# Optimization experiments

Hardware: AMD Instinct MI355X
Metric: run time of the kernel (lower is better)

The kernel has to match this reference:

```python
import jax, jax.numpy as jnp
import numpy as np

NUM_ANCHORS = 400_000
NUM_GTS = 64
NUM_CLASSES = 1
TOPK = 10
ALPHA = 1.0
BETA = 6.0
IMG = 640.0


def setup_inputs() -> dict:
    key = jax.random.key(0)
    k1, k2, k3, k4, k5, k6 = jax.random.split(key, 6)
    # anchor points uniformly over the image plane
    anc_points = jax.random.uniform(k1, (NUM_ANCHORS, 2), jnp.float32, 0.0, IMG)
    # predicted boxes: centered near the anchor point, valid xyxy
    pd_wh = jax.random.uniform(k2, (NUM_ANCHORS, 2), jnp.float32, 8.0, 96.0)
    pd_bboxes = jnp.concatenate([anc_points - pd_wh * 0.5, anc_points + pd_wh * 0.5], axis=-1)
    # predicted class scores in [0, 1] (post-sigmoid)
    pd_scores = jax.random.uniform(k3, (NUM_ANCHORS, NUM_CLASSES), jnp.float32)
    # GT boxes: random centers / sizes, valid xyxy
    gt_c = jax.random.uniform(k4, (NUM_GTS, 2), jnp.float32, 64.0, IMG - 64.0)
    gt_wh = jax.random.uniform(k5, (NUM_GTS, 2), jnp.float32, 16.0, 128.0)
    gt_bboxes = jnp.concatenate([gt_c - gt_wh * 0.5, gt_c + gt_wh * 0.5], axis=-1)
    gt_labels = jax.random.randint(k6, (NUM_GTS,), 0, NUM_CLASSES, dtype=jnp.int32)
    return {
        "pd_scores": pd_scores,
        "pd_bboxes": pd_bboxes,
        "anc_points": anc_points,
        "gt_labels": gt_labels,
        "gt_bboxes": gt_bboxes,
    }


def _box_iou(b1, b2):
    # b1: [A,4] xyxy, b2: [G,4] xyxy -> [A,G] pairwise IoU (torchvision box_iou math)
    lt = jnp.maximum(b1[:, None, :2], b2[None, :, :2])  # [A,G,2]
    rb = jnp.minimum(b1[:, None, 2:], b2[None, :, 2:])  # [A,G,2]
    wh = jnp.clip(rb - lt, 0.0)
    inter = wh[..., 0] * wh[..., 1]                      # [A,G]
    area1 = (b1[:, 2] - b1[:, 0]) * (b1[:, 3] - b1[:, 1])
    area2 = (b2[:, 2] - b2[:, 0]) * (b2[:, 3] - b2[:, 1])
    return inter / (area1[:, None] + area2[None, :] - inter)


def reference(pd_scores, pd_bboxes, anc_points, gt_labels, gt_bboxes):
    A = anc_points.shape[0]
    G = gt_bboxes.shape[0]
    # is anchor point inside each GT box -> [A,G] bool
    x, y = anc_points[:, 0:1], anc_points[:, 1:2]
    is_in_gts = ((x >= gt_bboxes[None, :, 0]) & (x <= gt_bboxes[None, :, 2]) &
                 (y >= gt_bboxes[None, :, 1]) & (y <= gt_bboxes[None, :, 3]))
    # Original gathers candidate anchors (inside >=1 GT) then computes metrics.
    # Equivalent dense form: non-candidates have is_in_gts row all-False so their
    # alignment metric is 0 for every GT and they are filtered by metric>0 below.
    iou = _box_iou(pd_bboxes, gt_bboxes)                         # [A,G]
    cls_scores = pd_scores[:, gt_labels]                          # [A,G]
    cls_scores = cls_scores * is_in_gts.astype(cls_scores.dtype)
    metric = (cls_scores ** ALPHA) * (iou ** BETA)                # [A,G]
    # per-GT top-k anchors by alignment metric
    _, topk_idx = jax.lax.top_k(metric.T, TOPK)                   # [G,k]
    topk_mask = jnp.zeros((A, G), dtype=bool)
    topk_mask = topk_mask.at[topk_idx.T, jnp.arange(G)[None, :]].set(True)
    topk_mask = topk_mask & (metric > 0)
    is_assigned = topk_mask.any(axis=1)                           # [A]
    best_gt = jnp.argmax(metric, axis=1)                          # [A]
    fg_mask = is_assigned
    assigned_gt_idx = jnp.where(fg_mask, best_gt, 0).astype(jnp.int32)
    return fg_mask, assigned_gt_idx
```

## Files before the change

### kernel.cpp

```cpp
#include <hip/hip_runtime.h>

#define NUM_A    400000
#define NUM_G    64
#define TOPK     10
#define CHUNKS   64
#define CHUNK_SZ (NUM_A / CHUNKS)
#define GGROUP   4
#define NGROUPS  (NUM_G / GGROUP)
#define CAP      768
#define SENT_I   0x7fffffff

__device__ __forceinline__ bool better(float m1, int a1, float m2, int a2) {
    return (m1 > m2) || ((m1 == m2) && (a1 < a2));
}

__device__ __forceinline__ float iou_metric(
    float px1, float py1, float px2, float py2, float parea, float score,
    float gx1, float gy1, float gx2, float gy2, float garea)
{
    float ltx = fmaxf(px1, gx1);
    float lty = fmaxf(py1, gy1);
    float rbx = fminf(px2, gx2);
    float rby = fminf(py2, gy2);
    float w = fmaxf(rbx - ltx, 0.0f);
    float h = fmaxf(rby - lty, 0.0f);
    float inter = w * h;
    float iou = inter / (parea + garea - inter);
    float iou2 = iou * iou;
    float iou6 = iou2 * iou2 * iou2;
    return score * iou6;
}

__device__ __forceinline__ void wave_max_pair(float& bv, int& bi) {
#pragma unroll
    for (int s = 1; s < 64; s <<= 1) {
        float ov = __shfl_xor(bv, s, 64);
        int   oi = __shfl_xor(bi, s, 64);
        if (better(ov, oi, bv, bi)) { bv = ov; bi = oi; }
    }
}

__global__ __launch_bounds__(256) void topk_partial_kernel(
    const float* __restrict__ pd_scores,
    const float* __restrict__ pd_bboxes,
    const float* __restrict__ anc_points,
    const float* __restrict__ gt_bboxes,
    float* __restrict__ pval,
    int*   __restrict__ pidx)
{
    const int c   = blockIdx.x;
    const int gg  = blockIdx.y;
    const int tid = threadIdx.x;
    const int g0  = gg * GGROUP;

    __shared__ int s_cnt[GGROUP];
    __shared__ int s_cand[GGROUP][CAP];

    if (tid < GGROUP) s_cnt[tid] = 0;

    float gx1[GGROUP], gy1[GGROUP], gx2[GGROUP], gy2[GGROUP];
#pragma unroll
    for (int j = 0; j < GGROUP; ++j) {
        float4 gb = ((const float4*)gt_bboxes)[g0 + j];
        gx1[j] = gb.x; gy1[j] = gb.y; gx2[j] = gb.z; gy2[j] = gb.w;
    }
    __syncthreads();

    const int p0 = c * (CHUNK_SZ / 2);
    const int p1 = p0 + CHUNK_SZ / 2;
    for (int p = p0 + tid; p < p1; p += 256) {
        float4 aq = ((const float4*)anc_points)[p];
        const int a2 = 2 * p;
#pragma unroll
        for (int j = 0; j < GGROUP; ++j) {
            bool in0 = (aq.x >= gx1[j]) && (aq.x <= gx2[j]) &&
                       (aq.y >= gy1[j]) && (aq.y <= gy2[j]);
            bool in1 = (aq.z >= gx1[j]) && (aq.z <= gx2[j]) &&
                       (aq.w >= gy1[j]) && (aq.w <= gy2[j]);
            if (in0) { int q = atomicAdd(&s_cnt[j], 1); if (q < CAP) s_cand[j][q] = a2; }
            if (in1) { int q = atomicAdd(&s_cnt[j], 1); if (q < CAP) s_cand[j][q] = a2 + 1; }
        }
    }
    __syncthreads();

    const int wj   = tid >> 6;
    const int lane = tid & 63;

    float4 gb = ((const float4*)gt_bboxes)[g0 + wj];
    const float garea = (gb.z - gb.x) * (gb.w - gb.y);
    const int n = min(s_cnt[wj], CAP);

    float tv[TOPK]; int ti[TOPK];
#pragma unroll
    for (int k = 0; k < TOPK; ++k) { tv[k] = 0.0f; ti[k] = SENT_I; }

    for (int i = lane; i < n; i += 64) {
        const int a = s_cand[wj][i];
        float4 pb = ((const float4*)pd_bboxes)[a];
        float sc = pd_scores[a];
        float parea = (pb.z - pb.x) * (pb.w - pb.y);
        float m = iou_metric(pb.x, pb.y, pb.z, pb.w, parea, sc,
                             gb.x, gb.y, gb.z, gb.w, garea);
        if (better(m, a, tv[TOPK - 1], ti[TOPK - 1])) {
#pragma unroll
            for (int k = TOPK - 1; k >= 1; --k) {
                bool gp = better(m, a, tv[k - 1], ti[k - 1]);
                bool gc = better(m, a, tv[k],     ti[k]);
                tv[k] = gp ? tv[k - 1] : (gc ? m : tv[k]);
                ti[k] = gp ? ti[k - 1] : (gc ? a : ti[k]);
            }
            if (better(m, a, tv[0], ti[0])) { tv[0] = m; ti[0] = a; }
        }
    }

    float outv = 0.0f; int outi = SENT_I;
#pragma unroll
    for (int k = 0; k < TOPK; ++k) {
        float bv = tv[0]; int bi = ti[0];
        wave_max_pair(bv, bi);
        bool win = (ti[0] == bi);
#pragma unroll
        for (int j = 0; j < TOPK - 1; ++j) {
            tv[j] = win ? tv[j + 1] : tv[j];
            ti[j] = win ? ti[j + 1] : ti[j];
        }
        if (win) { tv[TOPK - 1] = 0.0f; ti[TOPK - 1] = SENT_I; }
        if (lane == k) { outv = bv; outi = bi; }
    }
    if (lane < TOPK) {
        const int g = g0 + wj;
        pval[(g * CHUNKS + c) * TOPK + lane] = outv;
        pidx[(g * CHUNKS + c) * TOPK + lane] = outi;
    }
}

__global__ __launch_bounds__(64) void merge_assign_kernel(
    const float* __restrict__ pval,
    const int*   __restrict__ pidx,
    const float* __restrict__ pd_scores,
    const float* __restrict__ pd_bboxes,
    const float* __restrict__ anc_points,
    const float* __restrict__ gt_bboxes,
    int* __restrict__ out_fg,
    int* __restrict__ out_idx)
{
    const int g    = blockIdx.x;
    const int lane = threadIdx.x;

    float4 mygt = ((const float4*)gt_bboxes)[lane];
    float  myga = (mygt.z - mygt.x) * (mygt.w - mygt.y);

    float tv[TOPK]; int ti[TOPK];
    const float* pv = pval + (g * CHUNKS + lane) * TOPK;
    const int*   pi = pidx + (g * CHUNKS + lane) * TOPK;
#pragma unroll
    for (int k = 0; k < TOPK; ++k) { tv[k] = pv[k]; ti[k] = pi[k]; }

#pragma unroll
    for (int k = 0; k < TOPK; ++k) {
        float bv = tv[0]; int bi = ti[0];
        wave_max_pair(bv, bi);
        bool win = (ti[0] == bi);
#pragma unroll
        for (int j = 0; j < TOPK - 1; ++j) {
            tv[j] = win ? tv[j + 1] : tv[j];
            ti[j] = win ? ti[j + 1] : ti[j];
        }
        if (win) { tv[TOPK - 1] = 0.0f; ti[TOPK - 1] = SENT_I; }

        if (bv > 0.0f) {
            const int a = bi;
            float2 ap = ((const float2*)anc_points)[a];
            float4 pb = ((const float4*)pd_bboxes)[a];
            float  sc = pd_scores[a];
            float parea = (pb.z - pb.x) * (pb.w - pb.y);
            bool in = (ap.x >= mygt.x) && (ap.x <= mygt.z) &&
                      (ap.y >= mygt.y) && (ap.y <= mygt.w);
            float m = iou_metric(pb.x, pb.y, pb.z, pb.w, parea,
                                 in ? sc : 0.0f,
                                 mygt.x, mygt.y, mygt.z, mygt.w, myga);
            float av = m; int ag = lane;
#pragma unroll
            for (int s = 1; s < 64; s <<= 1) {
                float ov = __shfl_xor(av, s, 64);
                int   og = __shfl_xor(ag, s, 64);
                if ((ov > av) || ((ov == av) && (og < ag))) { av = ov; ag = og; }
            }
            if (lane == 0) { out_fg[a] = 1; out_idx[a] = ag; }
        }
    }
}

extern "C" void kernel_launch(void* const* d_in, const int* in_sizes, int n_in,
                              void* d_out, int out_size, void* d_ws, size_t ws_size,
                              hipStream_t stream) {
    const float* pd_scores  = (const float*)d_in[0];
    const float* pd_bboxes  = (const float*)d_in[1];
    const float* anc_points = (const float*)d_in[2];
    const float* gt_bboxes  = (const float*)d_in[4];

    const int npairs = NUM_G * CHUNKS * TOPK;
    float* pval = (float*)d_ws;
    int*   pidx = (int*)(pval + npairs);

    int* out_fg  = (int*)d_out;
    int* out_idx = out_fg + NUM_A;

    hipMemsetAsync(d_out, 0, 2 * NUM_A * sizeof(int), stream);

    dim3 g1(CHUNKS, NGROUPS);
    topk_partial_kernel<<<g1, 256, 0, stream>>>(
        pd_scores, pd_bboxes, anc_points, gt_bboxes, pval, pidx);
    merge_assign_kernel<<<NUM_G, 64, 0, stream>>>(
        pval, pidx, pd_scores, pd_bboxes, anc_points, gt_bboxes,
        out_fg, out_idx);
}
```

Measured before the change: 105.2 us.

## Fuse output zeroing into topk kernel, wave-aggregate candidate atomics, batch merge gathers

```diff
diff --git a/kernel.cpp b/kernel.cpp
--- a/kernel.cpp
+++ b/kernel.cpp
@@ -46,13 +46,19 @@
     const float* __restrict__ anc_points,
     const float* __restrict__ gt_bboxes,
     float* __restrict__ pval,
-    int*   __restrict__ pidx)
+    int*   __restrict__ pidx,
+    int*   __restrict__ out_zero)
 {
     const int c   = blockIdx.x;
     const int gg  = blockIdx.y;
     const int tid = threadIdx.x;
     const int g0  = gg * GGROUP;
 
+    {
+        const int t = (gg * CHUNKS + c) * 256 + tid;
+        if (t < (2 * NUM_A) / 4) ((int4*)out_zero)[t] = make_int4(0, 0, 0, 0);
+    }
+
     __shared__ int s_cnt[GGROUP];
     __shared__ int s_cand[GGROUP][CAP];
 
@@ -65,6 +71,9 @@
         gx1[j] = gb.x; gy1[j] = gb.y; gx2[j] = gb.z; gy2[j] = gb.w;
     }
     __syncthreads();
+
+    const int lane = tid & 63;
+    const unsigned long long lmlt = (1ull << lane) - 1ull;
 
     const int p0 = c * (CHUNK_SZ / 2);
     const int p1 = p0 + CHUNK_SZ / 2;
@@ -77,14 +86,28 @@
                        (aq.y >= gy1[j]) && (aq.y <= gy2[j]);
             bool in1 = (aq.z >= gx1[j]) && (aq.z <= gx2[j]) &&
                        (aq.w >= gy1[j]) && (aq.w <= gy2[j]);
-            if (in0) { int q = atomicAdd(&s_cnt[j], 1); if (q < CAP) s_cand[j][q] = a2; }
-            if (in1) { int q = atomicAdd(&s_cnt[j], 1); if (q < CAP) s_cand[j][q] = a2 + 1; }
+            unsigned long long b0 = __ballot(in0);
+            unsigned long long b1 = __ballot(in1);
+            if (b0 | b1) {
+                int c0  = __popcll(b0);
+                int tot = c0 + __popcll(b1);
+                int base;
+                if (lane == 0) base = atomicAdd(&s_cnt[j], tot);
+                base = __shfl(base, 0, 64);
+                if (in0) {
+                    int q = base + __popcll(b0 & lmlt);
+                    if (q < CAP) s_cand[j][q] = a2;
+                }
+                if (in1) {
+                    int q = base + c0 + __popcll(b1 & lmlt);
+                    if (q < CAP) s_cand[j][q] = a2 + 1;
+                }
+            }
         }
     }
     __syncthreads();
 
-    const int wj   = tid >> 6;
-    const int lane = tid & 63;
+    const int wj = tid >> 6;
 
     float4 gb = ((const float4*)gt_bboxes)[g0 + wj];
     const float garea = (gb.z - gb.x) * (gb.w - gb.y);
@@ -156,6 +179,7 @@
 #pragma unroll
     for (int k = 0; k < TOPK; ++k) { tv[k] = pv[k]; ti[k] = pi[k]; }
 
+    float outv = 0.0f; int outi = SENT_I;
 #pragma unroll
     for (int k = 0; k < TOPK; ++k) {
         float bv = tv[0]; int bi = ti[0];
@@ -167,17 +191,34 @@
             ti[j] = win ? ti[j + 1] : ti[j];
         }
         if (win) { tv[TOPK - 1] = 0.0f; ti[TOPK - 1] = SENT_I; }
-
-        if (bv > 0.0f) {
-            const int a = bi;
-            float2 ap = ((const float2*)anc_points)[a];
-            float4 pb = ((const float4*)pd_bboxes)[a];
-            float  sc = pd_scores[a];
-            float parea = (pb.z - pb.x) * (pb.w - pb.y);
-            bool in = (ap.x >= mygt.x) && (ap.x <= mygt.z) &&
-                      (ap.y >= mygt.y) && (ap.y <= mygt.w);
-            float m = iou_metric(pb.x, pb.y, pb.z, pb.w, parea,
-                                 in ? sc : 0.0f,
+        if (lane == k) { outv = bv; outi = bi; }
+    }
+
+    float wv[TOPK]; int wa[TOPK];
+#pragma unroll
+    for (int k = 0; k < TOPK; ++k) {
+        wv[k] = __shfl(outv, k, 64);
+        wa[k] = __shfl(outi, k, 64);
+    }
+
+    float4 pb[TOPK]; float sc[TOPK]; float2 ap[TOPK];
+#pragma unroll
+    for (int k = 0; k < TOPK; ++k) {
+        const int a = (wv[k] > 0.0f) ? wa[k] : 0;
+        pb[k] = ((const float4*)pd_bboxes)[a];
+        sc[k] = pd_scores[a];
+        ap[k] = ((const float2*)anc_points)[a];
+    }
+
+#pragma unroll
+    for (int k = 0; k < TOPK; ++k) {
+        if (wv[k] > 0.0f) {
+            const int a = wa[k];
+            float parea = (pb[k].z - pb[k].x) * (pb[k].w - pb[k].y);
+            bool in = (ap[k].x >= mygt.x) && (ap[k].x <= mygt.z) &&
+                      (ap[k].y >= mygt.y) && (ap[k].y <= mygt.w);
+            float m = iou_metric(pb[k].x, pb[k].y, pb[k].z, pb[k].w, parea,
+                                 in ? sc[k] : 0.0f,
                                  mygt.x, mygt.y, mygt.z, mygt.w, myga);
             float av = m; int ag = lane;
 #pragma unroll
@@ -206,11 +247,9 @@
     int* out_fg  = (int*)d_out;
     int* out_idx = out_fg + NUM_A;
 
-    hipMemsetAsync(d_out, 0, 2 * NUM_A * sizeof(int), stream);
-
     dim3 g1(CHUNKS, NGROUPS);
     topk_partial_kernel<<<g1, 256, 0, stream>>>(
-        pd_scores, pd_bboxes, anc_points, gt_bboxes, pval, pidx);
+        pd_scores, pd_bboxes, anc_points, gt_bboxes, pval, pidx, out_fg);
     merge_assign_kernel<<<NUM_G, 64, 0, stream>>>(
         pval, pidx, pd_scores, pd_bboxes, anc_points, gt_bboxes,
         out_fg, out_idx);
```

New measurement: 103.6 us. About the same (-1.6%).
